# Optimization experiments

Hardware: AMD Instinct MI355X
Metric: run time of the kernel (lower is better)

## Reference

```python
import jax, jax.numpy as jnp
import numpy as np

MU = 1.0  # opts.loss_type[1]


def setup_inputs() -> dict:
    key = jax.random.key(0)
    k1, k2 = jax.random.split(key)
    B, D, N = 8, 3, 4096
    srcs = jax.random.normal(k1, (B, D, N), dtype=jnp.float32)
    tgts = jax.random.normal(k2, (B, D, N), dtype=jnp.float32)
    return {"srcs": srcs, "tgts": tgts}


def reference(srcs, tgts):
    # [B, D, N] -> [B, N, D]
    s = jnp.transpose(srcs, (0, 2, 1))
    t = jnp.transpose(tgts, (0, 2, 1))
    # squared euclidean pairwise distances: ||s_i - t_j||^2, [B, N, M]
    s_sq = jnp.sum(s * s, axis=-1)          # [B, N]
    t_sq = jnp.sum(t * t, axis=-1)          # [B, M]
    cross = jnp.einsum('bnd,bmd->bnm', s, t)  # [B, N, M]
    P = s_sq[:, :, None] + t_sq[:, None, :] - 2.0 * cross
    # bidirectional chamfer mins
    d_tgt = jnp.min(P, axis=1)  # min over src points, [B, M]
    d_src = jnp.min(P, axis=2)  # min over tgt points, [B, N]
    distances = jnp.stack([d_tgt, d_src], axis=-1)  # [B, N, 2]
    # Geman-McClure robust penalty
    losses = (MU * distances / (distances + MU)).sum(axis=2).mean(axis=1).mean()
    return losses
```

## Files before the change

kernel.cpp:

```cpp
#include <hip/hip_runtime.h>


#define NPTS 4096
#define NB   8

typedef __attribute__((ext_vector_type(8))) short bf16x8;
typedef __attribute__((ext_vector_type(4))) float floatx4;

#define OFF_APACK_S 0u
#define OFF_APACK_T (1u << 20)
#define OFF_BPACK_S (2u << 20)
#define OFF_BPACK_T (3u << 20)
#define OFF_BSUM    (4u << 20)

union V16 { int4 i; bf16x8 h; };

__device__ __forceinline__ unsigned short f2bf(float f) {
    unsigned u = __float_as_uint(f);
    u += 0x7FFFu + ((u >> 16) & 1u);
    return (unsigned short)(u >> 16);
}
__device__ __forceinline__ float bf2f(unsigned short h) {
    return __uint_as_float(((unsigned)h) << 16);
}
__device__ __forceinline__ int pk(unsigned short lo, unsigned short hi) {
    return (int)((unsigned)lo | ((unsigned)hi << 16));
}

__device__ __forceinline__ void pack_point(const float* __restrict__ cloud,
                                           int b, int j, int gid,
                                           char* __restrict__ apack,
                                           char* __restrict__ bpack) {
    const unsigned short ONE = 0x3F80;
    const float* p = cloud + b * 3 * NPTS;
    const float x = p[j], y = p[NPTS + j], z = p[2 * NPTS + j];
    const unsigned short hx = f2bf(x), hy = f2bf(y), hz = f2bf(z);
    const unsigned short lx = f2bf(x - bf2f(hx));
    const unsigned short ly = f2bf(y - bf2f(hy));
    const unsigned short lz = f2bf(z - bf2f(hz));
    const unsigned short a0 = f2bf(-2.0f * bf2f(hx));
    const unsigned short a1 = f2bf(-2.0f * bf2f(hy));
    const unsigned short a2 = f2bf(-2.0f * bf2f(hz));
    const unsigned short m0 = f2bf(-2.0f * (x - bf2f(hx)));
    const unsigned short m1 = f2bf(-2.0f * (y - bf2f(hy)));
    const unsigned short m2 = f2bf(-2.0f * (z - bf2f(hz)));
    const float n2 = fmaf(z, z, fmaf(y, y, x * x));
    const unsigned short n2h = f2bf(n2);
    const unsigned short n2l = f2bf(n2 - bf2f(n2h));

    int4* Ap = (int4*)(apack + (size_t)gid * 32);
    Ap[0] = make_int4(pk(a0, a1), pk(a2, m0), pk(m1, m2), pk(a0, a1));
    Ap[1] = make_int4(pk(a2, n2h), pk(n2l, ONE), pk(ONE, 0), 0);

    int4* Bp = (int4*)(bpack + (size_t)gid * 32);
    Bp[0] = make_int4(pk(hx, hy), pk(hz, hx), pk(hy, hz), pk(lx, ly));
    Bp[1] = make_int4(pk(lz, ONE), pk(ONE, n2h), pk(n2l, 0), 0);
}

__global__ __launch_bounds__(256)
void transform_kernel(const float* __restrict__ srcs,
                      const float* __restrict__ tgts,
                      char* __restrict__ ws) {
    const int gid = blockIdx.x * 256 + threadIdx.x;
    const int dir = gid >> 15;
    const int rem = gid & 32767;
    const int b = rem >> 12, j = rem & 4095;
    if (dir == 0)
        pack_point(srcs, b, j, rem, ws + OFF_APACK_S, ws + OFF_BPACK_S);
    else
        pack_point(tgts, b, j, rem, ws + OFF_APACK_T, ws + OFF_BPACK_T);
}

__global__ __launch_bounds__(256, 2)
void chamfer_kernel(char* __restrict__ ws) {
    const int blk    = blockIdx.x;
    const int group  = blk & 15;
    const int dir    = group >> 3;
    const int b      = group & 7;
    const int stripe = blk >> 4;
    const int tid    = threadIdx.x;
    const int wave   = tid >> 6;
    const int lane   = tid & 63;
    const int l15    = lane & 15;
    const int quad   = lane >> 4;

    const char* Ap = ws + (dir == 0 ? OFF_APACK_S : OFF_APACK_T);
    const char* Bp = ws + (dir == 0 ? OFF_BPACK_T : OFF_BPACK_S);

    V16 av[4];
#pragma unroll
    for (int rt = 0; rt < 4; rt++)
        av[rt].i = *(const int4*)(Ap +
            (size_t)(b * NPTS + stripe * 64 + rt * 16 + l15) * 32 + (quad & 1) * 16);

    floatx4 rmin[4];
#pragma unroll
    for (int rt = 0; rt < 4; rt++)
        rmin[rt] = (floatx4){3.0e38f, 3.0e38f, 3.0e38f, 3.0e38f};
    const floatx4 zero = {0.0f, 0.0f, 0.0f, 0.0f};

    const int ct0 = wave * 64;
    const char* bbase = Bp + (size_t)(b * NPTS + ct0 * 16 + l15) * 32 + (quad & 1) * 16;

    V16 t0, t1, t2, t3;
    t0.i = *(const int4*)(bbase);
    t1.i = *(const int4*)(bbase + 512);
    t2.i = *(const int4*)(bbase + 1024);
    t3.i = *(const int4*)(bbase + 1536);

#pragma unroll
    for (int i = 0; i < 64; i += 4) {
        V16 n0, n1, n2, n3;
        n0.i = *(const int4*)(bbase + (size_t)((i + 4) & 63) * 512);
        n1.i = *(const int4*)(bbase + (size_t)((i + 5) & 63) * 512);
        n2.i = *(const int4*)(bbase + (size_t)((i + 6) & 63) * 512);
        n3.i = *(const int4*)(bbase + (size_t)((i + 7) & 63) * 512);
#pragma unroll
        for (int u = 0; u < 4; u++) {
            const bf16x8 bf = (u == 0 ? t0.h : u == 1 ? t1.h : u == 2 ? t2.h : t3.h);
#pragma unroll
            for (int rt = 0; rt < 4; rt++) {
                const floatx4 d =
                    __builtin_amdgcn_mfma_f32_16x16x32_bf16(av[rt].h, bf, zero, 0, 0, 0);
#pragma unroll
                for (int r = 0; r < 4; r++)
                    rmin[rt][r] = fminf(rmin[rt][r], d[r]);
            }
        }
        t0 = n0; t1 = n1; t2 = n2; t3 = n3;
    }

#pragma unroll
    for (int off = 1; off < 16; off <<= 1) {
#pragma unroll
        for (int rt = 0; rt < 4; rt++)
#pragma unroll
            for (int r = 0; r < 4; r++)
                rmin[rt][r] = fminf(rmin[rt][r], __shfl_xor(rmin[rt][r], off, 64));
    }
    __shared__ float sRow[4][64];
    if (l15 == 0) {
#pragma unroll
        for (int rt = 0; rt < 4; rt++)
#pragma unroll
            for (int r = 0; r < 4; r++)
                sRow[wave][rt * 16 + quad * 4 + r] = rmin[rt][r];
    }
    __syncthreads();
    if (tid < 64) {
        float m = fminf(fminf(sRow[0][tid], sRow[1][tid]),
                        fminf(sRow[2][tid], sRow[3][tid]));
        m = fmaxf(m * 0.5f, 0.0f);
        float g = m / (m + 1.0f);
#pragma unroll
        for (int off = 1; off < 64; off <<= 1)
            g += __shfl_xor(g, off, 64);
        if (tid == 0)
            ((float*)(ws + OFF_BSUM))[blk] = g;
    }
}

__global__ __launch_bounds__(256)
void finish_kernel(const char* __restrict__ ws, float* __restrict__ out) {
    const float* bsum = (const float*)(ws + OFF_BSUM);
    const int tid = threadIdx.x;
    float g = bsum[tid] + bsum[tid + 256] + bsum[tid + 512] + bsum[tid + 768];
#pragma unroll
    for (int off = 1; off < 64; off <<= 1)
        g += __shfl_xor(g, off, 64);
    __shared__ float sp[4];
    if ((tid & 63) == 0) sp[tid >> 6] = g;
    __syncthreads();
    if (tid == 0)
        out[0] = (sp[0] + sp[1] + sp[2] + sp[3]) * (1.0f / (NB * NPTS));
}

extern "C" void kernel_launch(void* const* d_in, const int* in_sizes, int n_in,
                              void* d_out, int out_size, void* d_ws, size_t ws_size,
                              hipStream_t stream) {
    const float* srcs = (const float*)d_in[0];
    const float* tgts = (const float*)d_in[1];
    float* out = (float*)d_out;
    char* ws = (char*)d_ws;

    transform_kernel<<<dim3(256), dim3(256), 0, stream>>>(srcs, tgts, ws);
    chamfer_kernel<<<dim3(1024), dim3(256), 0, stream>>>(ws);
    finish_kernel<<<dim3(1), dim3(256), 0, stream>>>(ws, out);
}
```

Before: 72.66 us.

## Compute both chamfer directions from one distance matrix pass with column partials

Instead of computing the src-to-tgt and tgt-to-src distance matrices separately, each block now computes the matrix once and takes both row minima and per-stripe column minima. The column minima are written to a workspace buffer and reduced by a new colreduce kernel before the final sum. This halves the MFMA work but adds extra shuffles, per-tile global stores of column partials (8 MB) and an additional kernel launch.

```diff
diff --git a/kernel.cpp b/kernel.cpp
--- a/kernel.cpp
+++ b/kernel.cpp
@@ -7,11 +7,10 @@
 typedef __attribute__((ext_vector_type(8))) short bf16x8;
 typedef __attribute__((ext_vector_type(4))) float floatx4;
 
-#define OFF_APACK_S 0u
-#define OFF_APACK_T (1u << 20)
-#define OFF_BPACK_S (2u << 20)
-#define OFF_BPACK_T (3u << 20)
-#define OFF_BSUM    (4u << 20)
+#define OFF_APACK 0u
+#define OFF_BPACK (1u << 20)
+#define OFF_CPART (2u << 20)
+#define OFF_BSUM  (10u << 20)
 
 union V16 { int4 i; bf16x8 h; };
 
@@ -27,17 +26,13 @@
     return (int)((unsigned)lo | ((unsigned)hi << 16));
 }
 
-__device__ __forceinline__ void pack_point(const float* __restrict__ cloud,
-                                           int b, int j, int gid,
-                                           char* __restrict__ apack,
-                                           char* __restrict__ bpack) {
+__device__ __forceinline__ void pack_A(const float* __restrict__ cloud,
+                                       int b, int j, int gid,
+                                       char* __restrict__ apack) {
     const unsigned short ONE = 0x3F80;
     const float* p = cloud + b * 3 * NPTS;
     const float x = p[j], y = p[NPTS + j], z = p[2 * NPTS + j];
     const unsigned short hx = f2bf(x), hy = f2bf(y), hz = f2bf(z);
-    const unsigned short lx = f2bf(x - bf2f(hx));
-    const unsigned short ly = f2bf(y - bf2f(hy));
-    const unsigned short lz = f2bf(z - bf2f(hz));
     const unsigned short a0 = f2bf(-2.0f * bf2f(hx));
     const unsigned short a1 = f2bf(-2.0f * bf2f(hy));
     const unsigned short a2 = f2bf(-2.0f * bf2f(hz));
@@ -47,11 +42,24 @@
     const float n2 = fmaf(z, z, fmaf(y, y, x * x));
     const unsigned short n2h = f2bf(n2);
     const unsigned short n2l = f2bf(n2 - bf2f(n2h));
-
     int4* Ap = (int4*)(apack + (size_t)gid * 32);
     Ap[0] = make_int4(pk(a0, a1), pk(a2, m0), pk(m1, m2), pk(a0, a1));
     Ap[1] = make_int4(pk(a2, n2h), pk(n2l, ONE), pk(ONE, 0), 0);
-
+}
+
+__device__ __forceinline__ void pack_B(const float* __restrict__ cloud,
+                                       int b, int j, int gid,
+                                       char* __restrict__ bpack) {
+    const unsigned short ONE = 0x3F80;
+    const float* p = cloud + b * 3 * NPTS;
+    const float x = p[j], y = p[NPTS + j], z = p[2 * NPTS + j];
+    const unsigned short hx = f2bf(x), hy = f2bf(y), hz = f2bf(z);
+    const unsigned short lx = f2bf(x - bf2f(hx));
+    const unsigned short ly = f2bf(y - bf2f(hy));
+    const unsigned short lz = f2bf(z - bf2f(hz));
+    const float n2 = fmaf(z, z, fmaf(y, y, x * x));
+    const unsigned short n2h = f2bf(n2);
+    const unsigned short n2l = f2bf(n2 - bf2f(n2h));
     int4* Bp = (int4*)(bpack + (size_t)gid * 32);
     Bp[0] = make_int4(pk(hx, hy), pk(hz, hx), pk(hy, hz), pk(lx, ly));
     Bp[1] = make_int4(pk(lz, ONE), pk(ONE, n2h), pk(n2l, 0), 0);
@@ -62,30 +70,25 @@
                       const float* __restrict__ tgts,
                       char* __restrict__ ws) {
     const int gid = blockIdx.x * 256 + threadIdx.x;
-    const int dir = gid >> 15;
-    const int rem = gid & 32767;
-    const int b = rem >> 12, j = rem & 4095;
-    if (dir == 0)
-        pack_point(srcs, b, j, rem, ws + OFF_APACK_S, ws + OFF_BPACK_S);
-    else
-        pack_point(tgts, b, j, rem, ws + OFF_APACK_T, ws + OFF_BPACK_T);
+    const int b = gid >> 12, j = gid & 4095;
+    pack_A(srcs, b, j, gid, ws + OFF_APACK);
+    pack_B(tgts, b, j, gid, ws + OFF_BPACK);
 }
 
 __global__ __launch_bounds__(256, 2)
 void chamfer_kernel(char* __restrict__ ws) {
     const int blk    = blockIdx.x;
-    const int group  = blk & 15;
-    const int dir    = group >> 3;
-    const int b      = group & 7;
-    const int stripe = blk >> 4;
+    const int b      = blk & 7;
+    const int stripe = blk >> 3;
     const int tid    = threadIdx.x;
     const int wave   = tid >> 6;
     const int lane   = tid & 63;
     const int l15    = lane & 15;
     const int quad   = lane >> 4;
 
-    const char* Ap = ws + (dir == 0 ? OFF_APACK_S : OFF_APACK_T);
-    const char* Bp = ws + (dir == 0 ? OFF_BPACK_T : OFF_BPACK_S);
+    const char* Ap = ws + OFF_APACK;
+    const char* Bp = ws + OFF_BPACK;
+    float* cpart = (float*)(ws + OFF_CPART) + (size_t)(b * 64 + stripe) * NPTS;
 
     V16 av[4];
 #pragma unroll
@@ -101,6 +104,7 @@
 
     const int ct0 = wave * 64;
     const char* bbase = Bp + (size_t)(b * NPTS + ct0 * 16 + l15) * 32 + (quad & 1) * 16;
+    float* cbase = cpart + ct0 * 16 + l15;
 
     V16 t0, t1, t2, t3;
     t0.i = *(const int4*)(bbase);
@@ -118,6 +122,7 @@
 #pragma unroll
         for (int u = 0; u < 4; u++) {
             const bf16x8 bf = (u == 0 ? t0.h : u == 1 ? t1.h : u == 2 ? t2.h : t3.h);
+            float colacc = 3.0e38f;
 #pragma unroll
             for (int rt = 0; rt < 4; rt++) {
                 const floatx4 d =
@@ -125,7 +130,13 @@
 #pragma unroll
                 for (int r = 0; r < 4; r++)
                     rmin[rt][r] = fminf(rmin[rt][r], d[r]);
+                colacc = fminf(colacc,
+                               fminf(fminf(d[0], d[1]), fminf(d[2], d[3])));
             }
+            colacc = fminf(colacc, __shfl_xor(colacc, 16, 64));
+            colacc = fminf(colacc, __shfl_xor(colacc, 32, 64));
+            if (quad == 0)
+                cbase[(i + u) * 16] = colacc;
         }
         t0 = n0; t1 = n1; t2 = n2; t3 = n3;
     }
@@ -161,10 +172,40 @@
 }
 
 __global__ __launch_bounds__(256)
-void finish_kernel(const char* __restrict__ ws, float* __restrict__ out) {
+void colreduce_kernel(char* __restrict__ ws) {
+    const int blk = blockIdx.x;
+    const int b   = blk & 7;
+    const int cc  = blk >> 3;
+    const int tid = threadIdx.x;
+    const float* cp = (const float*)(ws + OFF_CPART) +
+                      (size_t)b * 64 * NPTS + cc * 256 + tid;
+    float m0 = 3.0e38f, m1 = 3.0e38f, m2 = 3.0e38f, m3 = 3.0e38f;
+#pragma unroll 4
+    for (int s = 0; s < 64; s += 4) {
+        m0 = fminf(m0, cp[(size_t)(s + 0) * NPTS]);
+        m1 = fminf(m1, cp[(size_t)(s + 1) * NPTS]);
+        m2 = fminf(m2, cp[(size_t)(s + 2) * NPTS]);
+        m3 = fminf(m3, cp[(size_t)(s + 3) * NPTS]);
+    }
+    float m = fminf(fminf(m0, m1), fminf(m2, m3));
+    m = fmaxf(m * 0.5f, 0.0f);
+    float g = m / (m + 1.0f);
+#pragma unroll
+    for (int off = 1; off < 64; off <<= 1)
+        g += __shfl_xor(g, off, 64);
+    __shared__ float sp[4];
+    if ((tid & 63) == 0) sp[tid >> 6] = g;
+    __syncthreads();
+    if (tid == 0)
+        ((float*)(ws + OFF_BSUM))[512 + blk] = sp[0] + sp[1] + sp[2] + sp[3];
+}
+
+__global__ __launch_bounds__(256)
+void final_kernel(const char* __restrict__ ws, float* __restrict__ out) {
     const float* bsum = (const float*)(ws + OFF_BSUM);
     const int tid = threadIdx.x;
-    float g = bsum[tid] + bsum[tid + 256] + bsum[tid + 512] + bsum[tid + 768];
+    float g = bsum[tid] + bsum[tid + 256];
+    if (tid < 128) g += bsum[512 + tid];
 #pragma unroll
     for (int off = 1; off < 64; off <<= 1)
         g += __shfl_xor(g, off, 64);
@@ -183,7 +224,8 @@
     float* out = (float*)d_out;
     char* ws = (char*)d_ws;
 
-    transform_kernel<<<dim3(256), dim3(256), 0, stream>>>(srcs, tgts, ws);
-    chamfer_kernel<<<dim3(1024), dim3(256), 0, stream>>>(ws);
-    finish_kernel<<<dim3(1), dim3(256), 0, stream>>>(ws, out);
-}
+    transform_kernel<<<dim3(128), dim3(256), 0, stream>>>(srcs, tgts, ws);
+    chamfer_kernel<<<dim3(512), dim3(256), 0, stream>>>(ws);
+    colreduce_kernel<<<dim3(128), dim3(256), 0, stream>>>(ws);
+    final_kernel<<<dim3(1), dim3(256), 0, stream>>>(ws, out);
+}
```

Result: slower. 272.7 us (+275.2%).
